# Performance work log

Measured on AMD Instinct MI355X. Metric: run time of the kernel, lower is better.

The kernel has to match this reference:

```python
import jax, jax.numpy as jnp
import numpy as np

N_NODES = 20000
N_EDGES = 320000
F_IN = 4
PERIODS = 12
OUT_CH = 256   # A3TGCN out_channels (hard-coded in TemporalGNN)
HID = 128      # linear1 hidden
OUT_DIM = 12


def setup_inputs() -> dict:
    key = jax.random.key(0)
    ks = jax.random.split(key, 24)
    s = 0.1
    inp = {
        "x": jax.random.normal(ks[0], (N_NODES, F_IN, PERIODS), jnp.float32),
        "edge_index": jax.random.randint(ks[1], (2, N_EDGES), 0, N_NODES, dtype=jnp.int64),
        "edge_attr": jax.random.uniform(ks[2], (N_EDGES,), jnp.float32),
        # A3TGCN attention over periods
        "attention": jax.random.uniform(ks[3], (PERIODS,), jnp.float32),
        # TGCN: three GCNConv(in=F_IN, out=OUT_CH) weights+biases (z, r, h gates)
        "Wz": jax.random.normal(ks[4], (F_IN, OUT_CH), jnp.float32) * s,
        "bz": jnp.zeros((OUT_CH,), jnp.float32),
        "Wr": jax.random.normal(ks[5], (F_IN, OUT_CH), jnp.float32) * s,
        "br": jnp.zeros((OUT_CH,), jnp.float32),
        "Wh": jax.random.normal(ks[6], (F_IN, OUT_CH), jnp.float32) * s,
        "bh": jnp.zeros((OUT_CH,), jnp.float32),
        # TGCN: three Linear(2*OUT_CH -> OUT_CH) for the gates
        "Lzw": jax.random.normal(ks[7], (2 * OUT_CH, OUT_CH), jnp.float32) * s,
        "Lzb": jnp.zeros((OUT_CH,), jnp.float32),
        "Lrw": jax.random.normal(ks[8], (2 * OUT_CH, OUT_CH), jnp.float32) * s,
        "Lrb": jnp.zeros((OUT_CH,), jnp.float32),
        "Lhw": jax.random.normal(ks[9], (2 * OUT_CH, OUT_CH), jnp.float32) * s,
        "Lhb": jnp.zeros((OUT_CH,), jnp.float32),
        # MLP head
        "W1": jax.random.normal(ks[10], (OUT_CH, HID), jnp.float32) * s,
        "b1": jnp.zeros((HID,), jnp.float32),
        "W2": jax.random.normal(ks[11], (HID, OUT_DIM), jnp.float32) * s,
        "b2": jnp.zeros((OUT_DIM,), jnp.float32),
    }
    return inp


def _forward(x, edge_index, edge_attr, attention,
             Wz, bz, Wr, br, Wh, bh,
             Lzw, Lzb, Lrw, Lrb, Lhw, Lhb,
             W1, b1, W2, b2):
    N, F, T = x.shape
    src, dst = edge_index[0], edge_index[1]
    # GCN normalization with self-loops (PyG gcn_norm, fill_value=1):
    loop = jnp.arange(N)
    src_a = jnp.concatenate([src, loop])
    dst_a = jnp.concatenate([dst, loop])
    w_a = jnp.concatenate([edge_attr, jnp.ones((N,), x.dtype)])
    deg = jax.ops.segment_sum(w_a, dst_a, num_segments=N)
    dinv = jnp.where(deg > 0, jax.lax.rsqrt(deg), 0.0)
    norm = dinv[src_a] * w_a * dinv[dst_a]  # [E+N]

    def gcn(xt, W, b):
        xw = xt @ W                                   # [N, OUT_CH]
        msg = norm[:, None] * xw[src_a]               # [E+N, OUT_CH] (memory-bound gather)
        return jax.ops.segment_sum(msg, dst_a, num_segments=N) + b

    Hzero = jnp.zeros((N, OUT_CH), x.dtype)  # A3TGCN uses H=None -> zeros each period
    probs = jax.nn.softmax(attention)
    H_accum = jnp.zeros((N, OUT_CH), x.dtype)
    for t in range(T):  # fixed small number of periods
        xt = x[:, :, t]
        Z = jax.nn.sigmoid(jnp.concatenate([gcn(xt, Wz, bz), Hzero], axis=1) @ Lzw + Lzb)
        R = jax.nn.sigmoid(jnp.concatenate([gcn(xt, Wr, br), Hzero], axis=1) @ Lrw + Lrb)
        Htil = jnp.tanh(jnp.concatenate([gcn(xt, Wh, bh), Hzero * R], axis=1) @ Lhw + Lhb)
        Hnew = Z * Hzero + (1.0 - Z) * Htil
        H_accum = H_accum + probs[t] * Hnew

    out_hidden = H_accum
    h = jax.nn.relu(H_accum)
    h = jax.nn.relu(h @ W1 + b1)
    h = h @ W2 + b2
    return h, out_hidden


def reference(x, edge_index, edge_attr, attention,
              Wz, bz, Wr, br, Wh, bh,
              Lzw, Lzb, Lrw, Lrb, Lhw, Lhb,
              W1, b1, W2, b2):
    return _forward(x, edge_index, edge_attr, attention,
                    Wz, bz, Wr, br, Wh, bh,
                    Lzw, Lzb, Lrw, Lrb, Lhw, Lhb,
                    W1, b1, W2, b2)
```

## Files before the change

kernel.cpp:

```cpp
#include <hip/hip_runtime.h>
#include <math.h>

typedef float v2f __attribute__((ext_vector_type(2)));

#define NN 20000
#define NE 320000
#define TP 12
#define OC 256
#define HIDN 128
#define OD 12
#define FT 48
#define NPB 8
#define CAP 64
#define LOG2E 1.44269504088896340736f

#define NB_E    ((NE + 255) / 256)
#define NB_XT   ((NN * TP + 255) / 256)
#define NB_DINV ((NN + 255) / 256)
#define NB_W1T  16

#define OFF_CNT    0
#define OFF_DEG    (OFF_CNT + NN)
#define OFF_DINV   (OFF_DEG + NN)
#define OFF_MZ     (OFF_DINV + NN)
#define OFF_MH     (OFF_MZ + 4*OC)
#define OFF_CZ     (OFF_MH + 4*OC)
#define OFF_CH     (OFF_CZ + OC)
#define OFF_PROBS  (OFF_CH + OC)
#define OFF_W2T    (OFF_PROBS + 16)
#define OFF_W1T    (OFF_W2T + HIDN*OD)
#define OFF_ELL    (OFF_W1T + OC*HIDN)
#define OFF_XT     (OFF_ELL + 2*NN*CAP)
#define NEED_A_XT  ((size_t)(OFF_XT + NN*FT) * 4)
#define NEED_A     ((size_t)(OFF_ELL + 2*NN*CAP) * 4)

__device__ __forceinline__ int detect64(const void* ei) {
    const unsigned long long* p = (const unsigned long long*)ei;
    unsigned long long v = p[threadIdx.x & 63];
    return (__ballot(v < (unsigned long long)NN) == ~0ull) ? 1 : 0;
}

__device__ __forceinline__ int load_idx(const void* ei, int is64, long off) {
    return is64 ? (int)((const long long*)ei)[off] : ((const int*)ei)[off];
}

__device__ __forceinline__ float4 load_xrow(const float4* __restrict__ XT4,
                                            const float* __restrict__ x,
                                            int useXT, int n, int t) {
    if (useXT) return XT4[n * TP + t];
    const float* xb = x + n * FT + t;
    return make_float4(xb[0], xb[12], xb[24], xb[36]);
}

__global__ __launch_bounds__(256) void build_kernel(
    const void* ei, const float* __restrict__ w, const float* __restrict__ x,
    int* __restrict__ cnt, float* __restrict__ deg, float2* __restrict__ ell,
    float4* __restrict__ XT4, int useELL, int useXT) {
    int bid = blockIdx.x;
    if (bid < NB_E) {
        int is64 = detect64(ei);
        int e = bid * 256 + threadIdx.x;
        if (e < NE) {
            int src = load_idx(ei, is64, e);
            int dst = load_idx(ei, is64, (long)NE + e);
            float we = w[e];
            atomicAdd(&deg[dst], we);
            if (useELL) {
                int slot = atomicAdd(&cnt[dst], 1);
                if (slot < CAP)
                    ell[dst * CAP + slot] = make_float2(__int_as_float(src), we);
            }
        }
    } else if (useXT) {
        int idx = (bid - NB_E) * 256 + threadIdx.x;
        if (idx < NN * TP) {
            int n = idx / TP;
            int t = idx - n * TP;
            const float* xb = x + n * FT + t;
            XT4[idx] = make_float4(xb[0], xb[12], xb[24], xb[36]);
        }
    }
}

__global__ __launch_bounds__(256) void prep_kernel(
    const float* __restrict__ deg, float* __restrict__ dinv,
    const float* __restrict__ Wz, const float* __restrict__ bz,
    const float* __restrict__ Wh, const float* __restrict__ bh,
    const float* __restrict__ Lzw, const float* __restrict__ Lzb,
    const float* __restrict__ Lhw, const float* __restrict__ Lhb,
    const float* __restrict__ att,
    const float* __restrict__ W1, const float* __restrict__ W2,
    float* __restrict__ Mz, float* __restrict__ Mh,
    float* __restrict__ cz, float* __restrict__ ch,
    float* __restrict__ probs, float* __restrict__ W1T, float* __restrict__ W2T) {
    int bid = blockIdx.x;
    int tid = threadIdx.x;
    if (bid < NB_DINV) {
        int n = bid * 256 + tid;
        if (n < NN) dinv[n] = 1.0f / sqrtf(deg[n] + 1.0f);
    } else if (bid == NB_DINV) {
        int c = tid;
        float az0 = 0, az1 = 0, az2 = 0, az3 = 0, abz = 0;
        float ah0 = 0, ah1 = 0, ah2 = 0, ah3 = 0, abh = 0;
        for (int k = 0; k < OC; ++k) {
            float lz = Lzw[k * OC + c];
            float lh = Lhw[k * OC + c];
            az0 += Wz[k] * lz;
            az1 += Wz[OC + k] * lz;
            az2 += Wz[2 * OC + k] * lz;
            az3 += Wz[3 * OC + k] * lz;
            abz += bz[k] * lz;
            ah0 += Wh[k] * lh;
            ah1 += Wh[OC + k] * lh;
            ah2 += Wh[2 * OC + k] * lh;
            ah3 += Wh[3 * OC + k] * lh;
            abh += bh[k] * lh;
        }
        const float sz = LOG2E, sh2 = 2.0f * LOG2E;
        Mz[c] = az0 * sz; Mz[OC + c] = az1 * sz; Mz[2 * OC + c] = az2 * sz; Mz[3 * OC + c] = az3 * sz;
        Mh[c] = ah0 * sh2; Mh[OC + c] = ah1 * sh2; Mh[2 * OC + c] = ah2 * sh2; Mh[3 * OC + c] = ah3 * sh2;
        cz[c] = (abz + Lzb[c]) * sz;
        ch[c] = (abh + Lhb[c]) * sh2;
        if (c == 0) {
            float m = att[0];
            for (int t = 1; t < TP; ++t) m = fmaxf(m, att[t]);
            float sum = 0.0f, e[TP];
            for (int t = 0; t < TP; ++t) { e[t] = expf(att[t] - m); sum += e[t]; }
            for (int t = 0; t < TP; ++t) probs[t] = e[t] / sum;
        }
    } else if (bid == NB_DINV + 1) {
        if (tid < HIDN)
            for (int k = 0; k < OD; ++k) W2T[k * HIDN + tid] = W2[tid * OD + k];
    } else {
#pragma unroll
        for (int i = 0; i < 8; ++i) {
            int idx = (bid - (NB_DINV + 2)) * 2048 + i * 256 + tid;
            int k = idx >> 7;
            int j = idx & (HIDN - 1);
            W1T[j * OC + k] = W1[idx];
        }
    }
}

__global__ __launch_bounds__(256) void initP_kernel(
    const float* __restrict__ x, const float* __restrict__ dinv, float4* __restrict__ P4) {
    int idx = blockIdx.x * 256 + threadIdx.x;
    if (idx >= NN * TP) return;
    int n = idx / TP;
    int t = idx - n * TP;
    const float* xb = x + n * FT + t;
    float dn = dinv[n], s = dn * dn;
    P4[idx] = make_float4(s * xb[0], s * xb[12], s * xb[24], s * xb[36]);
}

__global__ __launch_bounds__(256) void scatterB_kernel(
    const void* ei, const float* __restrict__ w, const float* __restrict__ dinv,
    const float* __restrict__ x, float* __restrict__ P) {
    int idx = blockIdx.x * 256 + threadIdx.x;
    if (idx >= NE * FT) return;
    int is64 = detect64(ei);
    int e = idx / FT;
    int k = idx - e * FT;
    int src = load_idx(ei, is64, e);
    int dst = load_idx(ei, is64, (long)NE + e);
    float nrm = dinv[src] * w[e] * dinv[dst];
    int t = k >> 2, f = k & 3;
    atomicAdd(&P[dst * FT + k], nrm * x[src * FT + f * TP + t]);
}

__global__ __launch_bounds__(256) void main_kernel(
    const int* __restrict__ cnt, const float* __restrict__ dinv,
    const float2* __restrict__ ell, const float4* __restrict__ XT4,
    const float4* __restrict__ P4, const float* __restrict__ x,
    int useELL, int useXT,
    const float* __restrict__ Mz, const float* __restrict__ Mh,
    const float* __restrict__ cz, const float* __restrict__ ch,
    const float* __restrict__ probs,
    const float* __restrict__ W1T, const float* __restrict__ b1,
    const float* __restrict__ W2T, const float* __restrict__ b2,
    float* __restrict__ out) {
    int c = threadIdx.x;
    int nb = blockIdx.x * NPB;
    __shared__ float4 shp4[NPB * TP];
    __shared__ float shh[NPB][OC];
    __shared__ float shh1[NPB][HIDN + 4];

    v2f M0 = {Mz[c], Mh[c]};
    v2f M1 = {Mz[OC + c], Mh[OC + c]};
    v2f M2 = {Mz[2 * OC + c], Mh[2 * OC + c]};
    v2f M3 = {Mz[3 * OC + c], Mh[3 * OC + c]};
    v2f C0 = {cz[c], ch[c]};
    float pr[TP];
#pragma unroll
    for (int t = 0; t < TP; ++t) pr[t] = probs[t];

    if (useELL) {
        float4* part = (float4*)&shh[0][0];
        if (c < 2 * NPB * TP) {
            int q = c & 1;
            int i = c >> 1;
            int m = i / TP;
            int t = i - m * TP;
            int n = nb + m;
            float4 acc = make_float4(0.f, 0.f, 0.f, 0.f);
            if (q == 0) {
                float dn = dinv[n];
                float4 xv = load_xrow(XT4, x, useXT, n, t);
                acc = make_float4(dn * xv.x, dn * xv.y, dn * xv.z, dn * xv.w);
            }
            int cn = cnt[n];
            cn = cn < CAP ? cn : CAP;
            for (int e = q; e < cn; e += 2) {
                float2 r = ell[n * CAP + e];
                int s = __float_as_int(r.x);
                float nr = dinv[s] * r.y;
                float4 xs = load_xrow(XT4, x, useXT, s, t);
                acc.x = fmaf(nr, xs.x, acc.x);
                acc.y = fmaf(nr, xs.y, acc.y);
                acc.z = fmaf(nr, xs.z, acc.z);
                acc.w = fmaf(nr, xs.w, acc.w);
            }
            part[c] = acc;
        }
        __syncthreads();
        if (c < NPB * TP) {
            int m = c / TP;
            float dn = dinv[nb + m];
            float4 a = part[2 * c], b = part[2 * c + 1];
            shp4[c] = make_float4((a.x + b.x) * dn, (a.y + b.y) * dn,
                                  (a.z + b.z) * dn, (a.w + b.w) * dn);
        }
    } else {
        if (c < NPB * TP) shp4[c] = P4[nb * TP + c];
    }
    __syncthreads();

    for (int m = 0; m < NPB; ++m) {
        float hacc = 0.0f;
#pragma unroll
        for (int t = 0; t < TP; ++t) {
            float4 p = shp4[m * TP + t];
            v2f a = C0;
            a = __builtin_elementwise_fma((v2f){p.x, p.x}, M0, a);
            a = __builtin_elementwise_fma((v2f){p.y, p.y}, M1, a);
            a = __builtin_elementwise_fma((v2f){p.z, p.z}, M2, a);
            a = __builtin_elementwise_fma((v2f){p.w, p.w}, M3, a);
            float ea = __builtin_exp2f(a.x);
            float eb = __builtin_exp2f(a.y);
            float den = (1.0f + ea) * (1.0f + eb);
            float num = pr[t] * (eb - 1.0f);
            hacc = fmaf(num, __builtin_amdgcn_rcpf(den), hacc);
        }
        out[NN * OD + (nb + m) * OC + c] = hacc;
        shh[m][c] = fmaxf(hacc, 0.0f);
    }
    __syncthreads();

    {
        int j = c & (HIDN - 1);
        int m0 = (c >> 7) * 4;
        const float4* w1r = (const float4*)&W1T[j * OC];
        float s0 = 0, s1 = 0, s2 = 0, s3 = 0;
        for (int k4 = 0; k4 < OC / 4; ++k4) {
            float4 w = w1r[k4];
            float4 h0 = *(const float4*)&shh[m0 + 0][k4 * 4];
            float4 h1 = *(const float4*)&shh[m0 + 1][k4 * 4];
            float4 h2 = *(const float4*)&shh[m0 + 2][k4 * 4];
            float4 h3 = *(const float4*)&shh[m0 + 3][k4 * 4];
            s0 = fmaf(w.x, h0.x, fmaf(w.y, h0.y, fmaf(w.z, h0.z, fmaf(w.w, h0.w, s0))));
            s1 = fmaf(w.x, h1.x, fmaf(w.y, h1.y, fmaf(w.z, h1.z, fmaf(w.w, h1.w, s1))));
            s2 = fmaf(w.x, h2.x, fmaf(w.y, h2.y, fmaf(w.z, h2.z, fmaf(w.w, h2.w, s2))));
            s3 = fmaf(w.x, h3.x, fmaf(w.y, h3.y, fmaf(w.z, h3.z, fmaf(w.w, h3.w, s3))));
        }
        float bb = b1[j];
        shh1[m0 + 0][j] = fmaxf(s0 + bb, 0.0f);
        shh1[m0 + 1][j] = fmaxf(s1 + bb, 0.0f);
        shh1[m0 + 2][j] = fmaxf(s2 + bb, 0.0f);
        shh1[m0 + 3][j] = fmaxf(s3 + bb, 0.0f);
    }
    __syncthreads();

    if (c < NPB * OD) {
        int m = c / OD;
        int k = c - m * OD;
        const float4* w2r = (const float4*)&W2T[k * HIDN];
        const float4* hr  = (const float4*)&shh1[m][0];
        float a = b2[k];
        for (int j4 = 0; j4 < HIDN / 4; ++j4) {
            float4 w = w2r[j4];
            float4 h = hr[j4];
            a = fmaf(w.x, h.x, fmaf(w.y, h.y, fmaf(w.z, h.z, fmaf(w.w, h.w, a))));
        }
        out[(nb + m) * OD + k] = a;
    }
}

extern "C" void kernel_launch(void* const* d_in, const int* in_sizes, int n_in,
                              void* d_out, int out_size, void* d_ws, size_t ws_size,
                              hipStream_t stream) {
    const float* x   = (const float*)d_in[0];
    const void*  ei  = d_in[1];
    const float* ea  = (const float*)d_in[2];
    const float* att = (const float*)d_in[3];
    const float* Wz  = (const float*)d_in[4];
    const float* bz  = (const float*)d_in[5];
    const float* Wh  = (const float*)d_in[8];
    const float* bh  = (const float*)d_in[9];
    const float* Lzw = (const float*)d_in[10];
    const float* Lzb = (const float*)d_in[11];
    const float* Lhw = (const float*)d_in[14];
    const float* Lhb = (const float*)d_in[15];
    const float* W1  = (const float*)d_in[16];
    const float* b1  = (const float*)d_in[17];
    const float* W2  = (const float*)d_in[18];
    const float* b2  = (const float*)d_in[19];

    float* out = (float*)d_out;
    float* ws  = (float*)d_ws;

    int*    cnt   = (int*)(ws + OFF_CNT);
    float*  deg   = ws + OFF_DEG;
    float*  dinv  = ws + OFF_DINV;
    float*  Mz    = ws + OFF_MZ;
    float*  Mh    = ws + OFF_MH;
    float*  cz    = ws + OFF_CZ;
    float*  ch    = ws + OFF_CH;
    float*  probs = ws + OFF_PROBS;
    float*  W2T   = ws + OFF_W2T;
    float*  W1T   = ws + OFF_W1T;
    float2* ell   = (float2*)(ws + OFF_ELL);
    float*  P     = ws + OFF_ELL;
    float*  XT    = ws + OFF_XT;

    int useELL = (ws_size >= NEED_A) ? 1 : 0;
    int useXT  = (ws_size >= NEED_A_XT) ? 1 : 0;

    hipMemsetAsync(ws, 0, (size_t)OFF_DINV * sizeof(float), stream);
    build_kernel<<<NB_E + (useXT ? NB_XT : 0), 256, 0, stream>>>(
        ei, ea, x, cnt, deg, ell, (float4*)XT, useELL, useXT);
    prep_kernel<<<NB_DINV + 2 + NB_W1T, 256, 0, stream>>>(
        deg, dinv, Wz, bz, Wh, bh, Lzw, Lzb, Lhw, Lhb, att, W1, W2,
        Mz, Mh, cz, ch, probs, W1T, W2T);
    if (!useELL) {
        initP_kernel<<<(NN * TP + 255) / 256, 256, 0, stream>>>(x, dinv, (float4*)P);
        scatterB_kernel<<<(NE * FT + 255) / 256, 256, 0, stream>>>(ei, ea, dinv, x, P);
    }
    main_kernel<<<NN / NPB, 256, 0, stream>>>(cnt, dinv, ell, (const float4*)XT,
                                              (const float4*)P, x, useELL, useXT,
                                              Mz, Mh, cz, ch, probs,
                                              W1T, b1, W2T, b2, out);
}
```

Before: 204.4 us.

## Split fused main kernel into norm, gather, gate and MLP kernels

Breaks the monolithic per-node kernel into separate stages. A norm pass prescales ELL edge weights by both degree factors, a standalone gather kernel computes the aggregated features, a gate kernel handles 4 nodes per block, and an MLP kernel handles 16 nodes per block reading W1 directly, which removes the W1 transpose. The aim is better occupancy and load balance per stage and more weight reuse in the MLP. In exchange it adds kernel launches and round trips of the hidden state and aggregates through global memory.

```diff
diff --git a/kernel.cpp b/kernel.cpp
--- a/kernel.cpp
+++ b/kernel.cpp
@@ -10,14 +10,14 @@
 #define HIDN 128
 #define OD 12
 #define FT 48
-#define NPB 8
 #define CAP 64
+#define NG 4
+#define NM 16
 #define LOG2E 1.44269504088896340736f
 
 #define NB_E    ((NE + 255) / 256)
 #define NB_XT   ((NN * TP + 255) / 256)
 #define NB_DINV ((NN + 255) / 256)
-#define NB_W1T  16
 
 #define OFF_CNT    0
 #define OFF_DEG    (OFF_CNT + NN)
@@ -28,11 +28,11 @@
 #define OFF_CH     (OFF_CZ + OC)
 #define OFF_PROBS  (OFF_CH + OC)
 #define OFF_W2T    (OFF_PROBS + 16)
-#define OFF_W1T    (OFF_W2T + HIDN*OD)
-#define OFF_ELL    (OFF_W1T + OC*HIDN)
-#define OFF_XT     (OFF_ELL + 2*NN*CAP)
-#define NEED_A_XT  ((size_t)(OFF_XT + NN*FT) * 4)
-#define NEED_A     ((size_t)(OFF_ELL + 2*NN*CAP) * 4)
+#define OFF_ELL    (OFF_W2T + HIDN*OD)
+#define OFF_P      (OFF_ELL + 2*NN*CAP)
+#define OFF_XT     (OFF_P + NN*FT)
+#define NEED_ELL   ((size_t)(OFF_XT) * 4)
+#define NEED_XT    ((size_t)(OFF_XT + NN*FT) * 4)
 
 __device__ __forceinline__ int detect64(const void* ei) {
     const unsigned long long* p = (const unsigned long long*)ei;
@@ -88,11 +88,10 @@
     const float* __restrict__ Wh, const float* __restrict__ bh,
     const float* __restrict__ Lzw, const float* __restrict__ Lzb,
     const float* __restrict__ Lhw, const float* __restrict__ Lhb,
-    const float* __restrict__ att,
-    const float* __restrict__ W1, const float* __restrict__ W2,
+    const float* __restrict__ att, const float* __restrict__ W2,
     float* __restrict__ Mz, float* __restrict__ Mh,
     float* __restrict__ cz, float* __restrict__ ch,
-    float* __restrict__ probs, float* __restrict__ W1T, float* __restrict__ W2T) {
+    float* __restrict__ probs, float* __restrict__ W2T) {
     int bid = blockIdx.x;
     int tid = threadIdx.x;
     if (bid < NB_DINV) {
@@ -128,18 +127,55 @@
             for (int t = 0; t < TP; ++t) { e[t] = expf(att[t] - m); sum += e[t]; }
             for (int t = 0; t < TP; ++t) probs[t] = e[t] / sum;
         }
-    } else if (bid == NB_DINV + 1) {
+    } else {
         if (tid < HIDN)
             for (int k = 0; k < OD; ++k) W2T[k * HIDN + tid] = W2[tid * OD + k];
-    } else {
-#pragma unroll
-        for (int i = 0; i < 8; ++i) {
-            int idx = (bid - (NB_DINV + 2)) * 2048 + i * 256 + tid;
-            int k = idx >> 7;
-            int j = idx & (HIDN - 1);
-            W1T[j * OC + k] = W1[idx];
-        }
-    }
+    }
+}
+
+__global__ __launch_bounds__(256) void norm_kernel(
+    const int* __restrict__ cnt, const float* __restrict__ dinv, float2* __restrict__ ell) {
+    int idx = blockIdx.x * 256 + threadIdx.x;
+    int n = idx >> 6;
+    int slot = idx & (CAP - 1);
+    if (slot < cnt[n]) {
+        float2 r = ell[idx];
+        int s = __float_as_int(r.x);
+        ell[idx].y = r.y * dinv[s] * dinv[n];
+    }
+}
+
+__global__ __launch_bounds__(256) void gather_kernel(
+    const int* __restrict__ cnt, const float* __restrict__ dinv,
+    const float2* __restrict__ ell, const float4* __restrict__ XT4,
+    const float* __restrict__ x, int useXT, float4* __restrict__ P4) {
+    int idx = blockIdx.x * 256 + threadIdx.x;
+    int q = idx & 1;
+    int i = idx >> 1;
+    int n = i / TP;
+    int t = i - n * TP;
+    float4 acc = make_float4(0.f, 0.f, 0.f, 0.f);
+    if (q == 0) {
+        float dn = dinv[n];
+        float sw = dn * dn;
+        float4 xv = load_xrow(XT4, x, useXT, n, t);
+        acc = make_float4(sw * xv.x, sw * xv.y, sw * xv.z, sw * xv.w);
+    }
+    int cn = cnt[n];
+    cn = cn < CAP ? cn : CAP;
+    for (int e = q; e < cn; e += 2) {
+        float2 r = ell[n * CAP + e];
+        float4 xs = load_xrow(XT4, x, useXT, __float_as_int(r.x), t);
+        acc.x = fmaf(r.y, xs.x, acc.x);
+        acc.y = fmaf(r.y, xs.y, acc.y);
+        acc.z = fmaf(r.y, xs.z, acc.z);
+        acc.w = fmaf(r.y, xs.w, acc.w);
+    }
+    acc.x += __shfl_xor(acc.x, 1);
+    acc.y += __shfl_xor(acc.y, 1);
+    acc.z += __shfl_xor(acc.z, 1);
+    acc.w += __shfl_xor(acc.w, 1);
+    if (q == 0) P4[i] = acc;
 }
 
 __global__ __launch_bounds__(256) void initP_kernel(
@@ -168,23 +204,15 @@
     atomicAdd(&P[dst * FT + k], nrm * x[src * FT + f * TP + t]);
 }
 
-__global__ __launch_bounds__(256) void main_kernel(
-    const int* __restrict__ cnt, const float* __restrict__ dinv,
-    const float2* __restrict__ ell, const float4* __restrict__ XT4,
-    const float4* __restrict__ P4, const float* __restrict__ x,
-    int useELL, int useXT,
+__global__ __launch_bounds__(256) void gate_kernel(
+    const float4* __restrict__ P4,
     const float* __restrict__ Mz, const float* __restrict__ Mh,
     const float* __restrict__ cz, const float* __restrict__ ch,
-    const float* __restrict__ probs,
-    const float* __restrict__ W1T, const float* __restrict__ b1,
-    const float* __restrict__ W2T, const float* __restrict__ b2,
-    float* __restrict__ out) {
+    const float* __restrict__ probs, float* __restrict__ out) {
     int c = threadIdx.x;
-    int nb = blockIdx.x * NPB;
-    __shared__ float4 shp4[NPB * TP];
-    __shared__ float shh[NPB][OC];
-    __shared__ float shh1[NPB][HIDN + 4];
-
+    int nb = blockIdx.x * NG;
+    __shared__ float4 shp4[NG * TP];
+    if (c < NG * TP) shp4[c] = P4[nb * TP + c];
     v2f M0 = {Mz[c], Mh[c]};
     v2f M1 = {Mz[OC + c], Mh[OC + c]};
     v2f M2 = {Mz[2 * OC + c], Mh[2 * OC + c]};
@@ -193,49 +221,9 @@
     float pr[TP];
 #pragma unroll
     for (int t = 0; t < TP; ++t) pr[t] = probs[t];
-
-    if (useELL) {
-        float4* part = (float4*)&shh[0][0];
-        if (c < 2 * NPB * TP) {
-            int q = c & 1;
-            int i = c >> 1;
-            int m = i / TP;
-            int t = i - m * TP;
-            int n = nb + m;
-            float4 acc = make_float4(0.f, 0.f, 0.f, 0.f);
-            if (q == 0) {
-                float dn = dinv[n];
-                float4 xv = load_xrow(XT4, x, useXT, n, t);
-                acc = make_float4(dn * xv.x, dn * xv.y, dn * xv.z, dn * xv.w);
-            }
-            int cn = cnt[n];
-            cn = cn < CAP ? cn : CAP;
-            for (int e = q; e < cn; e += 2) {
-                float2 r = ell[n * CAP + e];
-                int s = __float_as_int(r.x);
-                float nr = dinv[s] * r.y;
-                float4 xs = load_xrow(XT4, x, useXT, s, t);
-                acc.x = fmaf(nr, xs.x, acc.x);
-                acc.y = fmaf(nr, xs.y, acc.y);
-                acc.z = fmaf(nr, xs.z, acc.z);
-                acc.w = fmaf(nr, xs.w, acc.w);
-            }
-            part[c] = acc;
-        }
-        __syncthreads();
-        if (c < NPB * TP) {
-            int m = c / TP;
-            float dn = dinv[nb + m];
-            float4 a = part[2 * c], b = part[2 * c + 1];
-            shp4[c] = make_float4((a.x + b.x) * dn, (a.y + b.y) * dn,
-                                  (a.z + b.z) * dn, (a.w + b.w) * dn);
-        }
-    } else {
-        if (c < NPB * TP) shp4[c] = P4[nb * TP + c];
-    }
     __syncthreads();
-
-    for (int m = 0; m < NPB; ++m) {
+#pragma unroll
+    for (int m = 0; m < NG; ++m) {
         float hacc = 0.0f;
 #pragma unroll
         for (int t = 0; t < TP; ++t) {
@@ -252,35 +240,48 @@
             hacc = fmaf(num, __builtin_amdgcn_rcpf(den), hacc);
         }
         out[NN * OD + (nb + m) * OC + c] = hacc;
-        shh[m][c] = fmaxf(hacc, 0.0f);
-    }
+    }
+}
+
+__global__ __launch_bounds__(256) void mlp_kernel(
+    const float* __restrict__ W1, const float* __restrict__ b1,
+    const float* __restrict__ W2T, const float* __restrict__ b2,
+    float* __restrict__ out) {
+    int c = threadIdx.x;
+    int nb = blockIdx.x * NM;
+    __shared__ float shh[NM][OC];
+    __shared__ float shh1[NM][HIDN + 4];
+#pragma unroll
+    for (int m = 0; m < NM; ++m)
+        shh[m][c] = fmaxf(out[NN * OD + (nb + m) * OC + c], 0.0f);
     __syncthreads();
 
     {
         int j = c & (HIDN - 1);
-        int m0 = (c >> 7) * 4;
-        const float4* w1r = (const float4*)&W1T[j * OC];
-        float s0 = 0, s1 = 0, s2 = 0, s3 = 0;
+        int m0 = (c >> 7) * 8;
+        float s[8];
+#pragma unroll
+        for (int i = 0; i < 8; ++i) s[i] = 0.0f;
         for (int k4 = 0; k4 < OC / 4; ++k4) {
-            float4 w = w1r[k4];
-            float4 h0 = *(const float4*)&shh[m0 + 0][k4 * 4];
-            float4 h1 = *(const float4*)&shh[m0 + 1][k4 * 4];
-            float4 h2 = *(const float4*)&shh[m0 + 2][k4 * 4];
-            float4 h3 = *(const float4*)&shh[m0 + 3][k4 * 4];
-            s0 = fmaf(w.x, h0.x, fmaf(w.y, h0.y, fmaf(w.z, h0.z, fmaf(w.w, h0.w, s0))));
-            s1 = fmaf(w.x, h1.x, fmaf(w.y, h1.y, fmaf(w.z, h1.z, fmaf(w.w, h1.w, s1))));
-            s2 = fmaf(w.x, h2.x, fmaf(w.y, h2.y, fmaf(w.z, h2.z, fmaf(w.w, h2.w, s2))));
-            s3 = fmaf(w.x, h3.x, fmaf(w.y, h3.y, fmaf(w.z, h3.z, fmaf(w.w, h3.w, s3))));
+            int kb = k4 * 4;
+            float w0 = W1[(kb + 0) * HIDN + j];
+            float w1 = W1[(kb + 1) * HIDN + j];
+            float w2 = W1[(kb + 2) * HIDN + j];
+            float w3 = W1[(kb + 3) * HIDN + j];
+#pragma unroll
+            for (int i = 0; i < 8; ++i) {
+                float4 h = *(const float4*)&shh[m0 + i][kb];
+                s[i] = fmaf(w0, h.x, fmaf(w1, h.y, fmaf(w2, h.z, fmaf(w3, h.w, s[i]))));
+            }
         }
         float bb = b1[j];
-        shh1[m0 + 0][j] = fmaxf(s0 + bb, 0.0f);
-        shh1[m0 + 1][j] = fmaxf(s1 + bb, 0.0f);
-        shh1[m0 + 2][j] = fmaxf(s2 + bb, 0.0f);
-        shh1[m0 + 3][j] = fmaxf(s3 + bb, 0.0f);
+#pragma unroll
+        for (int i = 0; i < 8; ++i)
+            shh1[m0 + i][j] = fmaxf(s[i] + bb, 0.0f);
     }
     __syncthreads();
 
-    if (c < NPB * OD) {
+    if (c < NM * OD) {
         int m = c / OD;
         int k = c - m * OD;
         const float4* w2r = (const float4*)&W2T[k * HIDN];
@@ -327,26 +328,27 @@
     float*  ch    = ws + OFF_CH;
     float*  probs = ws + OFF_PROBS;
     float*  W2T   = ws + OFF_W2T;
-    float*  W1T   = ws + OFF_W1T;
     float2* ell   = (float2*)(ws + OFF_ELL);
-    float*  P     = ws + OFF_ELL;
     float*  XT    = ws + OFF_XT;
 
-    int useELL = (ws_size >= NEED_A) ? 1 : 0;
-    int useXT  = (ws_size >= NEED_A_XT) ? 1 : 0;
+    int useELL = (ws_size >= NEED_ELL) ? 1 : 0;
+    int useXT  = (ws_size >= NEED_XT) ? 1 : 0;
+    float* P = useELL ? (ws + OFF_P) : (ws + OFF_ELL);
 
     hipMemsetAsync(ws, 0, (size_t)OFF_DINV * sizeof(float), stream);
     build_kernel<<<NB_E + (useXT ? NB_XT : 0), 256, 0, stream>>>(
         ei, ea, x, cnt, deg, ell, (float4*)XT, useELL, useXT);
-    prep_kernel<<<NB_DINV + 2 + NB_W1T, 256, 0, stream>>>(
-        deg, dinv, Wz, bz, Wh, bh, Lzw, Lzb, Lhw, Lhb, att, W1, W2,
-        Mz, Mh, cz, ch, probs, W1T, W2T);
-    if (!useELL) {
+    prep_kernel<<<NB_DINV + 2, 256, 0, stream>>>(
+        deg, dinv, Wz, bz, Wh, bh, Lzw, Lzb, Lhw, Lhb, att, W2,
+        Mz, Mh, cz, ch, probs, W2T);
+    if (useELL) {
+        norm_kernel<<<NN * CAP / 256, 256, 0, stream>>>(cnt, dinv, ell);
+        gather_kernel<<<2 * NN * TP / 256, 256, 0, stream>>>(
+            cnt, dinv, ell, (const float4*)XT, x, useXT, (float4*)P);
+    } else {
         initP_kernel<<<(NN * TP + 255) / 256, 256, 0, stream>>>(x, dinv, (float4*)P);
         scatterB_kernel<<<(NE * FT + 255) / 256, 256, 0, stream>>>(ei, ea, dinv, x, P);
     }
-    main_kernel<<<NN / NPB, 256, 0, stream>>>(cnt, dinv, ell, (const float4*)XT,
-                                              (const float4*)P, x, useELL, useXT,
-                                              Mz, Mh, cz, ch, probs,
-                                              W1T, b1, W2T, b2, out);
-}
+    gate_kernel<<<NN / NG, 256, 0, stream>>>((const float4*)P, Mz, Mh, cz, ch, probs, out);
+    mlp_kernel<<<NN / NM, 256, 0, stream>>>(W1, b1, W2T, b2, out);
+}
```

New measurement: 184.3 us. -9.8%, faster.
